# Performance work log

Measured on AMD Instinct MI355X. Metric: run time of the kernel, lower is better.

Reference implementation:

```python
import jax, jax.numpy as jnp
import numpy as np

# GlobalWorkspaceConfig constants (from init_kwargs)
DT_MS = 1.0
NMDA_TAU_MS = 100.0
IGNITE_THR = 0.58
WTA_INH = 0.85
K_SELECT = 2


def setup_inputs() -> dict:
    key = jax.random.key(0)
    k1, _ = jax.random.split(key)
    T, N = 8192, 4096
    # binary spikes with firing prob 0.7 so the EMA crosses ignite_thr=0.58
    spikes = (jax.random.uniform(k1, (T, N)) < 0.7).astype(jnp.float32)
    nmda0 = jnp.zeros((N,), jnp.float32)  # initial nmda_state buffer
    return {"spikes": spikes, "nmda0": nmda0}


def reference(spikes, nmda0):
    T, N = spikes.shape
    alpha = DT_MS / max(NMDA_TAU_MS, 1.0)  # 0.01

    # linear EMA recurrence: nmda_t = (1-alpha)*nmda_{t-1} + alpha*s_t
    def step(nmda, s_t):
        nmda = (1.0 - alpha) * nmda + alpha * s_t
        return nmda, nmda

    nmda_final, nmda_seq = jax.lax.scan(step, nmda0, spikes)  # nmda_seq: [T, N]

    # per-step ignition test: max over neurons vs threshold
    ignited = nmda_seq.max(axis=1) >= IGNITE_THR  # [T] bool

    # per-step top-k (k-WTA). wta_inh scaling kept for faithfulness.
    k = min(K_SELECT, N)
    scores = nmda_seq * WTA_INH
    _, idx = jax.lax.top_k(scores, k)  # [T, k]

    rows = jnp.arange(T)[:, None]
    ignite_mask = jnp.zeros((T, N), jnp.float32).at[rows, idx].set(1.0)
    ignite_mask = ignite_mask * ignited[:, None].astype(jnp.float32)

    # coverage = mean of the row mask = k/N when ignited, else 0
    coverage = jnp.where(ignited, jnp.float32(k) / jnp.float32(N), jnp.float32(0.0))

    return ignite_mask, coverage, nmda_final
```

## Files before the change

kernel.cpp:

```cpp
#include <hip/hip_runtime.h>
#include <cstdint>
#include <cstddef>

#define C_DECAY 0.99f
#define C_ALPHA 0.01f
#define C_THR   0.58f
#define C_WTA   0.85f

#define NPB   16
#define TILE  256

#define EMA_STEP(x) nmda = __fadd_rn(__fmul_rn(C_DECAY, nmda), __fmul_rn(C_ALPHA, (x)))

typedef const __attribute__((address_space(1))) void g_void;
typedef __attribute__((address_space(3))) void l_void;

__device__ __forceinline__ void gload_lds16(const float* g, float* l) {
  __builtin_amdgcn_global_load_lds((g_void*)g, (l_void*)l, 16, 0, 0);
}

__global__ __launch_bounds__(128)
void gw_phase1(const float* __restrict__ spikes, const float* __restrict__ nmda0,
               float* __restrict__ bnd, float* __restrict__ nmf,
               int T, int N, int Ls) {
  __shared__ float sb[2][TILE * NPB];
  const int w    = threadIdx.x >> 6;
  const int lane = threadIdx.x & 63;
  const int nblk = gridDim.x;
  const int bs   = (nblk % 8 == 0) ? ((blockIdx.x & 7) * (nblk >> 3) + (blockIdx.x >> 3))
                                   : (int)blockIdx.x;
  const int n0   = bs * NPB;
  const int ntiles = T / TILE;
  const int Lm1  = (1 << Ls) - 1;
  const int grow = lane >> 2;
  const int gc   = (lane & 3) * 4;

  if (w == 1) {
#pragma unroll
    for (int j = 0; j < TILE / 16; ++j)
      gload_lds16(spikes + (size_t)(j * 16 + grow) * N + n0 + gc, &sb[0][j * 256]);
  }
  __syncthreads();

  const int nn = lane & (NPB - 1);
  float nmda = 0.0f;
  if (w == 0) nmda = nmda0[n0 + nn];

  for (int tile = 0; tile < ntiles; ++tile) {
    const int cur = tile & 1;
    if (w == 0) {
      const float* buf = sb[cur];
      const int t0 = tile * TILE;
      float tA[16], tB[16];
#pragma unroll
      for (int i = 0; i < 16; ++i) tA[i] = buf[i * NPB + nn];
#pragma unroll
      for (int jp = 0; jp < TILE / 32; ++jp) {
#pragma unroll
        for (int i = 0; i < 16; ++i) tB[i] = buf[((2 * jp + 1) * 16 + i) * NPB + nn];
        { const int tb = t0 + 2 * jp * 16;
          if ((tb & Lm1) == 0 && lane < NPB) bnd[(size_t)(tb >> Ls) * N + n0 + lane] = nmda; }
#pragma unroll
        for (int i = 0; i < 16; ++i) EMA_STEP(tA[i]);
        if (jp < TILE / 32 - 1) {
#pragma unroll
          for (int i = 0; i < 16; ++i) tA[i] = buf[((2 * jp + 2) * 16 + i) * NPB + nn];
        }
        { const int tb = t0 + (2 * jp + 1) * 16;
          if ((tb & Lm1) == 0 && lane < NPB) bnd[(size_t)(tb >> Ls) * N + n0 + lane] = nmda; }
#pragma unroll
        for (int i = 0; i < 16; ++i) EMA_STEP(tB[i]);
      }
    } else if (tile + 1 < ntiles) {
      const int t0 = (tile + 1) * TILE;
#pragma unroll
      for (int j = 0; j < TILE / 16; ++j)
        gload_lds16(spikes + (size_t)(t0 + j * 16 + grow) * N + n0 + gc, &sb[cur ^ 1][j * 256]);
    }
    __syncthreads();
  }
  if (w == 0 && lane < NPB) nmf[n0 + lane] = nmda;
}

__device__ __forceinline__ void merge2(float& a1, int& i1, float& a2, int& i2,
                                       float b1, int j1, float b2, int j2) {
  const bool afirst = (a1 > b1) || (a1 == b1 && i1 < j1);
  const float w1 = afirst ? a1 : b1; const int wi1 = afirst ? i1 : j1;
  const float l1 = afirst ? b1 : a1; const int li1 = afirst ? j1 : i1;
  const float cc = afirst ? a2 : b2; const int ci  = afirst ? i2 : j2;
  const bool sfirst = (cc > l1) || (cc == l1 && ci < li1);
  a1 = w1; i1 = wi1;
  a2 = sfirst ? cc : l1; i2 = sfirst ? ci : li1;
}

__global__ __launch_bounds__(1024)
void gw_phase2(const float* __restrict__ spikes, const float* __restrict__ bnd,
               float* __restrict__ mask, float* __restrict__ cov,
               int T, int N, int L, float covval) {
  const int tid  = threadIdx.x;
  const int lane = tid & 63;
  const int wv   = tid >> 6;
  const int N4   = N >> 2;
  const float4* sp4 = (const float4*)spikes;
  float4* mk4 = (float4*)mask;

  __shared__ float ws1[16][16]; __shared__ int wi1s[16][16];
  __shared__ float ws2[16][16]; __shared__ int wi2s[16][16];
  __shared__ float wmx[16][16];
  __shared__ int gj1[16], gj2[16];

  float4 nm = ((const float4*)bnd)[(size_t)blockIdx.x * N4 + tid];
  const int base = tid * 4;
  const int t00  = blockIdx.x * L;

  for (int g = 0; g < L; g += 16) {
    const int tg = t00 + g;

#pragma unroll
    for (int r = 0; r < 16; ++r) {
      const float4 s = sp4[(size_t)(tg + r) * N4 + tid];

      nm.x = __fadd_rn(__fmul_rn(C_DECAY, nm.x), __fmul_rn(C_ALPHA, s.x));
      nm.y = __fadd_rn(__fmul_rn(C_DECAY, nm.y), __fmul_rn(C_ALPHA, s.y));
      nm.z = __fadd_rn(__fmul_rn(C_DECAY, nm.z), __fmul_rn(C_ALPHA, s.z));
      nm.w = __fadd_rn(__fmul_rn(C_DECAY, nm.w), __fmul_rn(C_ALPHA, s.w));

      const float c0s = __fmul_rn(nm.x, C_WTA);
      const float c1s = __fmul_rn(nm.y, C_WTA);
      const float c2s = __fmul_rn(nm.z, C_WTA);
      const float c3s = __fmul_rn(nm.w, C_WTA);

      float mx = fmaxf(fmaxf(nm.x, nm.y), fmaxf(nm.z, nm.w));

      float a1 = c0s; int i1 = base;
      float a2 = -__builtin_inff(); int i2 = 0x7fffffff;
      if (c1s > a1) { a2 = a1; i2 = i1; a1 = c1s; i1 = base + 1; }
      else if (c1s > a2) { a2 = c1s; i2 = base + 1; }
      if (c2s > a1) { a2 = a1; i2 = i1; a1 = c2s; i1 = base + 2; }
      else if (c2s > a2) { a2 = c2s; i2 = base + 2; }
      if (c3s > a1) { a2 = a1; i2 = i1; a1 = c3s; i1 = base + 3; }
      else if (c3s > a2) { a2 = c3s; i2 = base + 3; }

#pragma unroll
      for (int m = 1; m < 64; m <<= 1) {
        const float b1 = __shfl_xor(a1, m, 64); const int j1 = __shfl_xor(i1, m, 64);
        const float b2 = __shfl_xor(a2, m, 64); const int j2 = __shfl_xor(i2, m, 64);
        mx = fmaxf(mx, __shfl_xor(mx, m, 64));
        merge2(a1, i1, a2, i2, b1, j1, b2, j2);
      }
      if (lane == 0) { ws1[r][wv] = a1; wi1s[r][wv] = i1; ws2[r][wv] = a2; wi2s[r][wv] = i2; wmx[r][wv] = mx; }
    }
    __syncthreads();

    if (wv < 4) {
      const int row = wv * 4 + (lane >> 4);
      const int q = lane & 15;
      float a1 = ws1[row][q]; int i1 = wi1s[row][q];
      float a2 = ws2[row][q]; int i2 = wi2s[row][q];
      float gm = wmx[row][q];
#pragma unroll
      for (int m = 1; m < 16; m <<= 1) {
        const float b1 = __shfl_xor(a1, m, 64); const int j1 = __shfl_xor(i1, m, 64);
        const float b2 = __shfl_xor(a2, m, 64); const int j2 = __shfl_xor(i2, m, 64);
        gm = fmaxf(gm, __shfl_xor(gm, m, 64));
        merge2(a1, i1, a2, i2, b1, j1, b2, j2);
      }
      if ((lane & 15) == 0) {
        const int ig = (gm >= C_THR) ? 1 : 0;
        gj1[row] = ig ? i1 : -1;
        gj2[row] = ig ? i2 : -1;
        cov[tg + row] = ig ? covval : 0.0f;
      }
    }
    __syncthreads();

#pragma unroll
    for (int r = 0; r < 16; ++r) {
      const int j1 = gj1[r], j2 = gj2[r];
      float4 v;
      v.x = (j1 == base     || j2 == base)     ? 1.0f : 0.0f;
      v.y = (j1 == base + 1 || j2 == base + 1) ? 1.0f : 0.0f;
      v.z = (j1 == base + 2 || j2 == base + 2) ? 1.0f : 0.0f;
      v.w = (j1 == base + 3 || j2 == base + 3) ? 1.0f : 0.0f;
      mk4[(size_t)(tg + r) * N4 + tid] = v;
    }
    if (g + 16 < L) __syncthreads();
  }
}

extern "C" void kernel_launch(void* const* d_in, const int* in_sizes, int n_in,
                              void* d_out, int out_size, void* d_ws, size_t ws_size,
                              hipStream_t stream) {
  const float* spikes = (const float*)d_in[0];
  const float* nmda0  = (const float*)d_in[1];
  const int N = in_sizes[1];
  const int T = in_sizes[0] / N;

  float* out  = (float*)d_out;
  float* mask = out;
  float* cov  = out + (size_t)T * N;
  float* nmf  = cov + T;

  int Ls = 4;
  while (((size_t)(T >> Ls)) * (size_t)N * sizeof(float) > ws_size && Ls < 13) ++Ls;
  const int L = 1 << Ls;
  const int C = T >> Ls;
  float* bnd = (float*)d_ws;

  gw_phase1<<<N / NPB, 128, 0, stream>>>(spikes, nmda0, bnd, nmf, T, N, Ls);
  gw_phase2<<<C, N / 4, 0, stream>>>(spikes, bnd, mask, cov, T, N, L, 2.0f / (float)N);
}
```

Before: 138.2 us.

## Process eight neurons per thread in phase2 with prefetch and nontemporal mask stores

Phase2 blocks shrink to 512 threads, each owning two float4 groups (one in each half of the neuron range). This halves the number of wave-level top-2 shuffle reductions and the LDS partials per row. Spike rows are prefetched one step ahead in registers, and the mask is written with nontemporal stores to avoid cache pollution. The launch now hardcodes 512 threads, which silently assumes N equals 4096, and the extra registers may reduce occupancy.

```diff
diff --git a/kernel.cpp b/kernel.cpp
--- a/kernel.cpp
+++ b/kernel.cpp
@@ -14,6 +14,7 @@
 
 typedef const __attribute__((address_space(1))) void g_void;
 typedef __attribute__((address_space(3))) void l_void;
+typedef float f32x4 __attribute__((ext_vector_type(4)));
 
 __device__ __forceinline__ void gload_lds16(const float* g, float* l) {
   __builtin_amdgcn_global_load_lds((g_void*)g, (l_void*)l, 16, 0, 0);
@@ -93,7 +94,11 @@
   a2 = sfirst ? cc : l1; i2 = sfirst ? ci : li1;
 }
 
-__global__ __launch_bounds__(1024)
+#define LOCAL_TOP2(c, idx)                                         \
+  if ((c) > a1) { a2 = a1; i2 = i1; a1 = (c); i1 = (idx); }        \
+  else if ((c) > a2) { a2 = (c); i2 = (idx); }
+
+__global__ __launch_bounds__(512)
 void gw_phase2(const float* __restrict__ spikes, const float* __restrict__ bnd,
                float* __restrict__ mask, float* __restrict__ cov,
                int T, int N, int L, float covval) {
@@ -101,45 +106,57 @@
   const int lane = tid & 63;
   const int wv   = tid >> 6;
   const int N4   = N >> 2;
+  const int half = N4 >> 1;
   const float4* sp4 = (const float4*)spikes;
-  float4* mk4 = (float4*)mask;
-
-  __shared__ float ws1[16][16]; __shared__ int wi1s[16][16];
-  __shared__ float ws2[16][16]; __shared__ int wi2s[16][16];
-  __shared__ float wmx[16][16];
+  f32x4* mk4 = (f32x4*)mask;
+
+  __shared__ float ws1[16][8]; __shared__ int wi1s[16][8];
+  __shared__ float ws2[16][8]; __shared__ int wi2s[16][8];
+  __shared__ float wmx[16][8];
   __shared__ int gj1[16], gj2[16];
 
-  float4 nm = ((const float4*)bnd)[(size_t)blockIdx.x * N4 + tid];
-  const int base = tid * 4;
-  const int t00  = blockIdx.x * L;
+  float4 nmA = ((const float4*)bnd)[(size_t)blockIdx.x * N4 + tid];
+  float4 nmB = ((const float4*)bnd)[(size_t)blockIdx.x * N4 + tid + half];
+  const int baseA = tid * 4;
+  const int baseB = baseA + (N >> 1);
+  const int t00   = blockIdx.x * L;
 
   for (int g = 0; g < L; g += 16) {
     const int tg = t00 + g;
 
+    float4 pA[2], pB[2];
+    pA[0] = sp4[(size_t)tg * N4 + tid];
+    pB[0] = sp4[(size_t)tg * N4 + tid + half];
 #pragma unroll
     for (int r = 0; r < 16; ++r) {
-      const float4 s = sp4[(size_t)(tg + r) * N4 + tid];
-
-      nm.x = __fadd_rn(__fmul_rn(C_DECAY, nm.x), __fmul_rn(C_ALPHA, s.x));
-      nm.y = __fadd_rn(__fmul_rn(C_DECAY, nm.y), __fmul_rn(C_ALPHA, s.y));
-      nm.z = __fadd_rn(__fmul_rn(C_DECAY, nm.z), __fmul_rn(C_ALPHA, s.z));
-      nm.w = __fadd_rn(__fmul_rn(C_DECAY, nm.w), __fmul_rn(C_ALPHA, s.w));
-
-      const float c0s = __fmul_rn(nm.x, C_WTA);
-      const float c1s = __fmul_rn(nm.y, C_WTA);
-      const float c2s = __fmul_rn(nm.z, C_WTA);
-      const float c3s = __fmul_rn(nm.w, C_WTA);
-
-      float mx = fmaxf(fmaxf(nm.x, nm.y), fmaxf(nm.z, nm.w));
-
-      float a1 = c0s; int i1 = base;
+      if (r < 15) {
+        pA[(r + 1) & 1] = sp4[(size_t)(tg + r + 1) * N4 + tid];
+        pB[(r + 1) & 1] = sp4[(size_t)(tg + r + 1) * N4 + tid + half];
+      }
+      const float4 s  = pA[r & 1];
+      const float4 s2 = pB[r & 1];
+
+      nmA.x = __fadd_rn(__fmul_rn(C_DECAY, nmA.x), __fmul_rn(C_ALPHA, s.x));
+      nmA.y = __fadd_rn(__fmul_rn(C_DECAY, nmA.y), __fmul_rn(C_ALPHA, s.y));
+      nmA.z = __fadd_rn(__fmul_rn(C_DECAY, nmA.z), __fmul_rn(C_ALPHA, s.z));
+      nmA.w = __fadd_rn(__fmul_rn(C_DECAY, nmA.w), __fmul_rn(C_ALPHA, s.w));
+      nmB.x = __fadd_rn(__fmul_rn(C_DECAY, nmB.x), __fmul_rn(C_ALPHA, s2.x));
+      nmB.y = __fadd_rn(__fmul_rn(C_DECAY, nmB.y), __fmul_rn(C_ALPHA, s2.y));
+      nmB.z = __fadd_rn(__fmul_rn(C_DECAY, nmB.z), __fmul_rn(C_ALPHA, s2.z));
+      nmB.w = __fadd_rn(__fmul_rn(C_DECAY, nmB.w), __fmul_rn(C_ALPHA, s2.w));
+
+      const float cA0 = __fmul_rn(nmA.x, C_WTA), cA1 = __fmul_rn(nmA.y, C_WTA);
+      const float cA2 = __fmul_rn(nmA.z, C_WTA), cA3 = __fmul_rn(nmA.w, C_WTA);
+      const float cB0 = __fmul_rn(nmB.x, C_WTA), cB1 = __fmul_rn(nmB.y, C_WTA);
+      const float cB2 = __fmul_rn(nmB.z, C_WTA), cB3 = __fmul_rn(nmB.w, C_WTA);
+      float mx = fmaxf(fmaxf(fmaxf(nmA.x, nmA.y), fmaxf(nmA.z, nmA.w)),
+                       fmaxf(fmaxf(nmB.x, nmB.y), fmaxf(nmB.z, nmB.w)));
+
+      float a1 = cA0; int i1 = baseA;
       float a2 = -__builtin_inff(); int i2 = 0x7fffffff;
-      if (c1s > a1) { a2 = a1; i2 = i1; a1 = c1s; i1 = base + 1; }
-      else if (c1s > a2) { a2 = c1s; i2 = base + 1; }
-      if (c2s > a1) { a2 = a1; i2 = i1; a1 = c2s; i1 = base + 2; }
-      else if (c2s > a2) { a2 = c2s; i2 = base + 2; }
-      if (c3s > a1) { a2 = a1; i2 = i1; a1 = c3s; i1 = base + 3; }
-      else if (c3s > a2) { a2 = c3s; i2 = base + 3; }
+      LOCAL_TOP2(cA1, baseA + 1); LOCAL_TOP2(cA2, baseA + 2); LOCAL_TOP2(cA3, baseA + 3);
+      LOCAL_TOP2(cB0, baseB);     LOCAL_TOP2(cB1, baseB + 1);
+      LOCAL_TOP2(cB2, baseB + 2); LOCAL_TOP2(cB3, baseB + 3);
 
 #pragma unroll
       for (int m = 1; m < 64; m <<= 1) {
@@ -152,20 +169,20 @@
     }
     __syncthreads();
 
-    if (wv < 4) {
-      const int row = wv * 4 + (lane >> 4);
-      const int q = lane & 15;
+    if (wv < 2) {
+      const int row = wv * 8 + (lane >> 3);
+      const int q = lane & 7;
       float a1 = ws1[row][q]; int i1 = wi1s[row][q];
       float a2 = ws2[row][q]; int i2 = wi2s[row][q];
       float gm = wmx[row][q];
 #pragma unroll
-      for (int m = 1; m < 16; m <<= 1) {
+      for (int m = 1; m < 8; m <<= 1) {
         const float b1 = __shfl_xor(a1, m, 64); const int j1 = __shfl_xor(i1, m, 64);
         const float b2 = __shfl_xor(a2, m, 64); const int j2 = __shfl_xor(i2, m, 64);
         gm = fmaxf(gm, __shfl_xor(gm, m, 64));
         merge2(a1, i1, a2, i2, b1, j1, b2, j2);
       }
-      if ((lane & 15) == 0) {
+      if ((lane & 7) == 0) {
         const int ig = (gm >= C_THR) ? 1 : 0;
         gj1[row] = ig ? i1 : -1;
         gj2[row] = ig ? i2 : -1;
@@ -177,12 +194,17 @@
 #pragma unroll
     for (int r = 0; r < 16; ++r) {
       const int j1 = gj1[r], j2 = gj2[r];
-      float4 v;
-      v.x = (j1 == base     || j2 == base)     ? 1.0f : 0.0f;
-      v.y = (j1 == base + 1 || j2 == base + 1) ? 1.0f : 0.0f;
-      v.z = (j1 == base + 2 || j2 == base + 2) ? 1.0f : 0.0f;
-      v.w = (j1 == base + 3 || j2 == base + 3) ? 1.0f : 0.0f;
-      mk4[(size_t)(tg + r) * N4 + tid] = v;
+      f32x4 v, u;
+      v.x = (j1 == baseA     || j2 == baseA)     ? 1.0f : 0.0f;
+      v.y = (j1 == baseA + 1 || j2 == baseA + 1) ? 1.0f : 0.0f;
+      v.z = (j1 == baseA + 2 || j2 == baseA + 2) ? 1.0f : 0.0f;
+      v.w = (j1 == baseA + 3 || j2 == baseA + 3) ? 1.0f : 0.0f;
+      u.x = (j1 == baseB     || j2 == baseB)     ? 1.0f : 0.0f;
+      u.y = (j1 == baseB + 1 || j2 == baseB + 1) ? 1.0f : 0.0f;
+      u.z = (j1 == baseB + 2 || j2 == baseB + 2) ? 1.0f : 0.0f;
+      u.w = (j1 == baseB + 3 || j2 == baseB + 3) ? 1.0f : 0.0f;
+      __builtin_nontemporal_store(v, &mk4[(size_t)(tg + r) * N4 + tid]);
+      __builtin_nontemporal_store(u, &mk4[(size_t)(tg + r) * N4 + tid + half]);
     }
     if (g + 16 < L) __syncthreads();
   }
@@ -208,5 +230,5 @@
   float* bnd = (float*)d_ws;
 
   gw_phase1<<<N / NPB, 128, 0, stream>>>(spikes, nmda0, bnd, nmf, T, N, Ls);
-  gw_phase2<<<C, N / 4, 0, stream>>>(spikes, bnd, mask, cov, T, N, L, 2.0f / (float)N);
-}
+  gw_phase2<<<C, 512, 0, stream>>>(spikes, bnd, mask, cov, T, N, L, 2.0f / (float)N);
+}
```

Result: faster. 117.0 us (-15.3%).
